# Kernel tuning notes

Hardware: AMD Instinct MI355X
Metric: run time of the kernel (lower is better)

Reference implementation:

```python
import jax, jax.numpy as jnp
import numpy as np

N_NODES = 50000
N_EDGES = 800000
N_GRAPHS = 1024
H = 128          # hidden_dim
L = 5            # n_conv_layers
NODE_IN = 4
EDGE_IN = 41
N_TARGETS = 3
EPS = 1e-5


def _ln(x, g, b):
    m = jnp.mean(x, axis=-1, keepdims=True)
    v = jnp.var(x, axis=-1, keepdims=True)
    return (x - m) / jnp.sqrt(v + EPS) * g + b


def setup_inputs() -> dict:
    key = jax.random.key(0)
    ks = jax.random.split(key, 24)
    w = lambda k, shp: (jax.random.normal(k, shp, dtype=jnp.float32) * 0.05)
    inp = {
        "atom_fea": jax.random.normal(ks[0], (N_NODES, NODE_IN), dtype=jnp.float32),
        "nbr_fea": jax.random.normal(ks[1], (N_EDGES, EDGE_IN), dtype=jnp.float32),
        "nbr_idx": jax.random.randint(ks[2], (N_EDGES, 2), 0, N_NODES, dtype=jnp.int32),
        "batch_mapping": jnp.sort(jax.random.randint(ks[3], (N_NODES,), 0, N_GRAPHS, dtype=jnp.int32)),
        # node embedding: Linear(4->H) + LayerNorm + SiLU
        "emb_w": w(ks[4], (NODE_IN, H)), "emb_b": jnp.zeros((H,), jnp.float32),
        "emb_ln_g": jnp.ones((H,), jnp.float32), "emb_ln_b": jnp.zeros((H,), jnp.float32),
        # edge embedding: Linear(41->H) + SiLU
        "edge_w": w(ks[5], (EDGE_IN, H)), "edge_b": jnp.zeros((H,), jnp.float32),
        # conv layers: Linear(2H->2H), SiLU, Linear(2H->H), SiLU; stacked over L
        "conv_w1": w(ks[6], (L, 2 * H, 2 * H)), "conv_b1": jnp.zeros((L, 2 * H), jnp.float32),
        "conv_w2": w(ks[7], (L, 2 * H, H)), "conv_b2": jnp.zeros((L, H), jnp.float32),
        "ln_g": jnp.ones((L, H), jnp.float32), "ln_b": jnp.zeros((L, H), jnp.float32),
        # output head
        "out_w1": w(ks[8], (H, H)), "out_b1": jnp.zeros((H,), jnp.float32),
        "out_w2": w(ks[9], (H, H // 2)), "out_b2": jnp.zeros((H // 2,), jnp.float32),
        "out_w3": w(ks[10], (H // 2, N_TARGETS)), "out_b3": jnp.zeros((N_TARGETS,), jnp.float32),
    }
    return inp


def reference(atom_fea, nbr_fea, nbr_idx, batch_mapping,
              emb_w, emb_b, emb_ln_g, emb_ln_b, edge_w, edge_b,
              conv_w1, conv_b1, conv_w2, conv_b2, ln_g, ln_b,
              out_w1, out_b1, out_w2, out_b2, out_w3, out_b3):
    silu = jax.nn.silu
    # embeddings (dropout is eval-mode identity)
    x = silu(_ln(atom_fea @ emb_w + emb_b, emb_ln_g, emb_ln_b))      # [N, H]
    e = silu(nbr_fea @ edge_w + edge_b)                               # [E, H]
    src, dst = nbr_idx[:, 0], nbr_idx[:, 1]
    n = x.shape[0]
    # per-node incoming edge counts (same every layer)
    cnt = jax.ops.segment_sum(jnp.ones_like(dst, dtype=x.dtype), dst, num_segments=n)
    cnt = jnp.clip(cnt, 1.0)[:, None]
    for i in range(L):
        m = jnp.concatenate([x[src], e], axis=1)                      # [E, 2H] gather
        m = silu(m @ conv_w1[i] + conv_b1[i])                         # [E, 2H]
        m = silu(m @ conv_w2[i] + conv_b2[i])                         # [E, H]
        aggr = jax.ops.segment_sum(m, dst, num_segments=n) / cnt      # scatter-mean
        x = _ln(x + aggr, ln_g[i], ln_b[i])                           # residual + LN
    # graph-level mean pooling
    gcnt = jax.ops.segment_sum(jnp.ones((n,), x.dtype), batch_mapping, num_segments=N_GRAPHS)
    gcnt = jnp.clip(gcnt, 1.0)[:, None]
    crystal = jax.ops.segment_sum(x, batch_mapping, num_segments=N_GRAPHS) / gcnt  # [G, H]
    h = silu(crystal @ out_w1 + out_b1)
    h = silu(h @ out_w2 + out_b2)
    return h @ out_w3 + out_b3                                        # [G, n_targets]
```

## Files before the change

### kernel.cpp

```cpp
#include <hip/hip_runtime.h>
#include <hip/hip_bf16.h>
#include <math.h>

#define N_NODES 50000
#define N_EDGES 800000
#define N_GRAPHS 1024
#define HD 128
#define NLAYERS 5
#define EDGE_IN 41
#define NT 3
#define LN_EPS 1e-5f

typedef unsigned int uint;
typedef unsigned short ushort;
typedef __attribute__((ext_vector_type(8))) short short8;
typedef __attribute__((ext_vector_type(4))) float f32x4;

__device__ __forceinline__ float silu_f(float v) {
    return v * __builtin_amdgcn_rcpf(1.0f + __expf(-v));
}

__device__ __forceinline__ ushort f2bf(float f) {
    uint u = __float_as_uint(f);
    u = u + 0x7FFFu + ((u >> 16) & 1u);
    return (ushort)(u >> 16);
}

__device__ __forceinline__ short8 ld16(const ushort* p) {
    union { int4 i; short8 s; } u;
    u.i = *(const int4*)p;
    return u.s;
}

__device__ __forceinline__ f32x4 mfma16(short8 a, short8 b, f32x4 c) {
    return __builtin_amdgcn_mfma_f32_16x16x32_bf16(a, b, c, 0, 0, 0);
}

__device__ __forceinline__ void wave_lds_fence() {
    __asm__ volatile("s_waitcnt lgkmcnt(0)" ::: "memory");
}

__device__ __forceinline__ void cp16(const ushort* g, ushort* l) {
    __builtin_amdgcn_global_load_lds(
        (const __attribute__((address_space(1))) unsigned int*)g,
        (__attribute__((address_space(3))) unsigned int*)l, 16, 0, 0);
}

__device__ __forceinline__ void stage4k(ushort* lds, const ushort* g, int w, int L) {
#pragma unroll
    for (int i = 0; i < 2; ++i) {
        int f = w * 1024 + i * 512;
        cp16(g + f + L * 8, lds + f);
    }
}

__global__ void k_zero(float* __restrict__ p, int n) {
    int i = blockIdx.x * 256 + threadIdx.x;
    if (i < n) p[i] = 0.0f;
}

__global__ void k_swz_w1(const float* __restrict__ w1, ushort* __restrict__ w1s) {
    int i = blockIdx.x * 256 + threadIdx.x;
    int l = i >> 16;
    int r = i & 65535;
    int j = r & 7, L = (r >> 3) & 63, s = (r >> 9) & 7, c = (r >> 12) & 15;
    int k = 32 * s + ((L >> 4) & 3) * 8 + j;
    int n = 16 * c + (L & 15);
    w1s[i] = f2bf(w1[(size_t)l * 65536 + k * 256 + n]);
}
__global__ void k_swz_w2(const float* __restrict__ w2, ushort* __restrict__ w2s) {
    int i = blockIdx.x * 256 + threadIdx.x;
    int l = i >> 15;
    int r = i & 32767;
    int j = r & 7, L = (r >> 3) & 63, t = (r >> 9) & 7, s2 = (r >> 12) & 7;
    int k = 32 * s2 + ((L >> 4) & 3) * 8 + j;
    int n = 16 * t + (L & 15);
    w2s[i] = f2bf(w2[(size_t)l * 32768 + k * 128 + n]);
}

__global__ __launch_bounds__(128) void k_node_embed(
    const float* __restrict__ atom, const float* __restrict__ w,
    const float* __restrict__ b, const float* __restrict__ g,
    const float* __restrict__ bet, float* __restrict__ x, ushort* __restrict__ x_bf)
{
    int node = blockIdx.x;
    int h = threadIdx.x;
    float4 a = *(const float4*)(atom + (size_t)node * 4);
    float acc = b[h] + a.x * w[h] + a.y * w[HD + h] + a.z * w[2 * HD + h] + a.w * w[3 * HD + h];
    __shared__ float s1[2], s2[2];
    float sum = acc, sq = acc * acc;
    for (int off = 32; off > 0; off >>= 1) { sum += __shfl_down(sum, off); sq += __shfl_down(sq, off); }
    int wid = h >> 6, lane = h & 63;
    if (lane == 0) { s1[wid] = sum; s2[wid] = sq; }
    __syncthreads();
    float m = (s1[0] + s1[1]) * (1.0f / 128.0f);
    float v = (s2[0] + s2[1]) * (1.0f / 128.0f) - m * m;
    float y = (acc - m) * rsqrtf(v + LN_EPS) * g[h] + bet[h];
    y = silu_f(y);
    x[(size_t)node * HD + h] = y;
    x_bf[(size_t)node * HD + h] = f2bf(y);
}

#define ETILE 32
__global__ __launch_bounds__(128) void k_edge_embed(
    const float* __restrict__ fea, const float* __restrict__ w,
    const float* __restrict__ b, ushort* __restrict__ e_bf)
{
    __shared__ float sf[ETILE][EDGE_IN + 1];
    int e0 = blockIdx.x * ETILE;
    int tid = threadIdx.x;
    for (int i = tid; i < ETILE * EDGE_IN; i += 128) {
        int m = i / EDGE_IN, k = i % EDGE_IN;
        sf[m][k] = fea[(size_t)(e0 + m) * EDGE_IN + k];
    }
    __syncthreads();
    float bb = b[tid];
    float acc[ETILE];
#pragma unroll
    for (int m = 0; m < ETILE; m++) acc[m] = bb;
    for (int k = 0; k < EDGE_IN; k++) {
        float wk = w[k * HD + tid];
#pragma unroll
        for (int m = 0; m < ETILE; m++) acc[m] += sf[m][k] * wk;
    }
#pragma unroll
    for (int m = 0; m < ETILE; m++)
        e_bf[(size_t)(e0 + m) * HD + tid] = f2bf(silu_f(acc[m]));
}

__global__ void k_count(const int* __restrict__ nbr_idx, float* __restrict__ cnt) {
    int i = blockIdx.x * 256 + threadIdx.x;
    if (i < N_EDGES) atomicAdd(&cnt[nbr_idx[2 * i + 1]], 1.0f);
}
__global__ void k_gcount(const int* __restrict__ bm, float* __restrict__ gcnt) {
    int i = blockIdx.x * 256 + threadIdx.x;
    if (i < N_NODES) atomicAdd(&gcnt[bm[i]], 1.0f);
}

#define M1CP 40
__global__ __launch_bounds__(256) void k_conv_mfma(
    const ushort* __restrict__ x_bf, const ushort* __restrict__ e_bf,
    const int* __restrict__ nbr_idx,
    const ushort* __restrict__ w1s, const float* __restrict__ cb1,
    const ushort* __restrict__ w2s, const float* __restrict__ cb2,
    float* __restrict__ aggr)
{
    __shared__ __align__(16) ushort sW1[2][4096];
    __shared__ __align__(16) ushort sW2[2][4096];
    __shared__ __align__(16) ushort sM1[4][16 * M1CP];
    __shared__ int sDst[64];

    int tid = threadIdx.x;
    int w = tid >> 6;
    int L = tid & 63;
    int m = L & 15;
    int quad = L >> 4;
    int e0 = blockIdx.x * 64 + w * 16;

    if (L < 16) sDst[w * 16 + L] = nbr_idx[2 * (e0 + L) + 1];
    int src = nbr_idx[2 * (e0 + m)];

    const ushort* xr = x_bf + (size_t)src * HD + quad * 8;
    const ushort* er = e_bf + (size_t)(e0 + m) * HD + quad * 8;
    short8 af[8];
#pragma unroll
    for (int s = 0; s < 4; ++s) af[s] = ld16(xr + 32 * s);
#pragma unroll
    for (int s = 0; s < 4; ++s) af[4 + s] = ld16(er + 32 * s);

    f32x4 acc2[8];
#pragma unroll
    for (int t = 0; t < 8; ++t)
#pragma unroll
        for (int r = 0; r < 4; ++r) acc2[t][r] = 0.0f;

    ushort* sm = sM1[w];

    stage4k(sW1[0], w1s, w, L);
    stage4k(sW2[0], w2s, w, L);

    for (int p = 0; p < 16; ++p) {
        __syncthreads();
        if (p < 15) stage4k(sW1[(p + 1) & 1], w1s + (p + 1) * 4096, w, L);
        if ((p & 1) && (p >> 1) < 7)
            stage4k(sW2[((p >> 1) + 1) & 1], w2s + ((p >> 1) + 1) * 4096, w, L);

        f32x4 a1;
#pragma unroll
        for (int r = 0; r < 4; ++r) a1[r] = 0.0f;
        const ushort* wb = sW1[p & 1] + L * 8;
#pragma unroll
        for (int s = 0; s < 8; ++s)
            a1 = mfma16(af[s], ld16(wb + s * 512), a1);

        float bv = cb1[p * 16 + m];
        int hb = (p & 1) * 16;
#pragma unroll
        for (int r = 0; r < 4; ++r)
            sm[(quad * 4 + r) * M1CP + hb + m] = f2bf(silu_f(a1[r] + bv));

        if (p & 1) {
            wave_lds_fence();
            short8 a2 = ld16(sm + m * M1CP + quad * 8);
            const ushort* w2p = sW2[(p >> 1) & 1] + L * 8;
#pragma unroll
            for (int t = 0; t < 8; ++t)
                acc2[t] = mfma16(a2, ld16(w2p + t * 512), acc2[t]);
            wave_lds_fence();
        }
    }

#pragma unroll
    for (int t = 0; t < 8; ++t) {
        float bv = cb2[t * 16 + m];
#pragma unroll
        for (int r = 0; r < 4; ++r) {
            int dst = sDst[w * 16 + quad * 4 + r];
            atomicAdd(aggr + (size_t)dst * HD + t * 16 + m, silu_f(acc2[t][r] + bv));
        }
    }
}

__global__ __launch_bounds__(128) void k_post(
    const float* __restrict__ aggr, const float* __restrict__ cnt,
    const float* __restrict__ g, const float* __restrict__ bet,
    float* __restrict__ x, ushort* __restrict__ x_bf)
{
    int node = blockIdx.x;
    int h = threadIdx.x;
    float inv = __builtin_amdgcn_rcpf(fmaxf(cnt[node], 1.0f));
    float acc = x[(size_t)node * HD + h] + aggr[(size_t)node * HD + h] * inv;
    __shared__ float s1[2], s2[2];
    float sum = acc, sq = acc * acc;
    for (int off = 32; off > 0; off >>= 1) { sum += __shfl_down(sum, off); sq += __shfl_down(sq, off); }
    int wid = h >> 6, lane = h & 63;
    if (lane == 0) { s1[wid] = sum; s2[wid] = sq; }
    __syncthreads();
    float m = (s1[0] + s1[1]) * (1.0f / 128.0f);
    float v = (s2[0] + s2[1]) * (1.0f / 128.0f) - m * m;
    float y = (acc - m) * rsqrtf(v + LN_EPS) * g[h] + bet[h];
    x[(size_t)node * HD + h] = y;
    x_bf[(size_t)node * HD + h] = f2bf(y);
}

__global__ __launch_bounds__(128) void k_gaggr(
    const float* __restrict__ x, const int* __restrict__ bm,
    float* __restrict__ crystal)
{
    int node = blockIdx.x;
    int h = threadIdx.x;
    atomicAdd(&crystal[(size_t)bm[node] * HD + h], x[(size_t)node * HD + h]);
}

__global__ __launch_bounds__(128) void k_readout(
    const float* __restrict__ crystal, const float* __restrict__ gcnt,
    const float* __restrict__ w1, const float* __restrict__ b1,
    const float* __restrict__ w2, const float* __restrict__ b2,
    const float* __restrict__ w3, const float* __restrict__ b3,
    float* __restrict__ out)
{
    int gph = blockIdx.x;
    int t = threadIdx.x;
    __shared__ float sc[HD], sh1[HD], sh2[64];
    float inv = __builtin_amdgcn_rcpf(fmaxf(gcnt[gph], 1.0f));
    sc[t] = crystal[(size_t)gph * HD + t] * inv;
    __syncthreads();
    float acc = b1[t];
    for (int k = 0; k < HD; k++) acc += sc[k] * w1[k * HD + t];
    sh1[t] = silu_f(acc);
    __syncthreads();
    if (t < 64) {
        float a2 = b2[t];
        for (int k = 0; k < HD; k++) a2 += sh1[k] * w2[k * 64 + t];
        sh2[t] = silu_f(a2);
    }
    __syncthreads();
    if (t < NT) {
        float a3 = b3[t];
        for (int k = 0; k < 64; k++) a3 += sh2[k] * w3[k * NT + t];
        out[(size_t)gph * NT + t] = a3;
    }
}

extern "C" void kernel_launch(void* const* d_in, const int* in_sizes, int n_in,
                              void* d_out, int out_size, void* d_ws, size_t ws_size,
                              hipStream_t stream)
{
    const float* atom_fea = (const float*)d_in[0];
    const float* nbr_fea  = (const float*)d_in[1];
    const int*   nbr_idx  = (const int*)d_in[2];
    const int*   bm       = (const int*)d_in[3];
    const float* emb_w    = (const float*)d_in[4];
    const float* emb_b    = (const float*)d_in[5];
    const float* emb_ln_g = (const float*)d_in[6];
    const float* emb_ln_b = (const float*)d_in[7];
    const float* edge_w   = (const float*)d_in[8];
    const float* edge_b   = (const float*)d_in[9];
    const float* conv_w1  = (const float*)d_in[10];
    const float* conv_b1  = (const float*)d_in[11];
    const float* conv_w2  = (const float*)d_in[12];
    const float* conv_b2  = (const float*)d_in[13];
    const float* ln_g     = (const float*)d_in[14];
    const float* ln_b     = (const float*)d_in[15];
    const float* out_w1   = (const float*)d_in[16];
    const float* out_b1   = (const float*)d_in[17];
    const float* out_w2   = (const float*)d_in[18];
    const float* out_b2   = (const float*)d_in[19];
    const float* out_w3   = (const float*)d_in[20];
    const float* out_b3   = (const float*)d_in[21];
    float* out = (float*)d_out;

    char* base = (char*)d_ws;
    size_t off = 0;
    auto alloc = [&](size_t bytes) -> char* {
        char* p = base + off;
        off = (off + bytes + 255) & ~(size_t)255;
        return p;
    };
    float*  xbuf    = (float*) alloc((size_t)N_NODES * HD * 4);
    float*  aggr    = (float*) alloc((size_t)N_NODES * HD * 4);
    float*  cnt     = (float*) alloc((size_t)N_NODES * 4);
    float*  crystal = (float*) alloc((size_t)N_GRAPHS * HD * 4);
    float*  gcnt    = (float*) alloc((size_t)N_GRAPHS * 4);
    ushort* x_bf    = (ushort*)alloc((size_t)N_NODES * HD * 2);
    ushort* e_bf    = (ushort*)alloc((size_t)N_EDGES * HD * 2);
    ushort* w1s     = (ushort*)alloc((size_t)NLAYERS * 65536 * 2);
    ushort* w2s     = (ushort*)alloc((size_t)NLAYERS * 32768 * 2);

    k_swz_w1<<<(NLAYERS * 65536) / 256, 256, 0, stream>>>(conv_w1, w1s);
    k_swz_w2<<<(NLAYERS * 32768) / 256, 256, 0, stream>>>(conv_w2, w2s);

    int zn = N_NODES + N_GRAPHS * HD + N_GRAPHS + 128;
    k_zero<<<(zn + 255) / 256, 256, 0, stream>>>(cnt, zn);

    k_node_embed<<<N_NODES, 128, 0, stream>>>(atom_fea, emb_w, emb_b, emb_ln_g, emb_ln_b, xbuf, x_bf);
    k_edge_embed<<<N_EDGES / ETILE, 128, 0, stream>>>(nbr_fea, edge_w, edge_b, e_bf);
    k_count<<<N_EDGES / 256, 256, 0, stream>>>(nbr_idx, cnt);
    k_gcount<<<(N_NODES + 255) / 256, 256, 0, stream>>>(bm, gcnt);

    for (int l = 0; l < NLAYERS; ++l) {
        k_zero<<<(N_NODES * HD) / 256, 256, 0, stream>>>(aggr, N_NODES * HD);
        k_conv_mfma<<<N_EDGES / 64, 256, 0, stream>>>(
            x_bf, e_bf, nbr_idx,
            w1s + (size_t)l * 65536, conv_b1 + (size_t)l * 256,
            w2s + (size_t)l * 32768, conv_b2 + (size_t)l * 128,
            aggr);
        k_post<<<N_NODES, 128, 0, stream>>>(aggr, cnt, ln_g + (size_t)l * HD, ln_b + (size_t)l * HD, xbuf, x_bf);
    }

    k_gaggr<<<N_NODES, 128, 0, stream>>>(xbuf, bm, crystal);
    k_readout<<<N_GRAPHS, 128, 0, stream>>>(crystal, gcnt, out_w1, out_b1, out_w2, out_b2, out_w3, out_b3, out);
}
```

Baseline: 2.794 ms.

## Process 32 edges per wave to reuse weight fragments; fold aggr zeroing into post

Each wave now handles two 16-edge tiles, so every weight fragment loaded from LDS feeds two MFMAs. This halves LDS weight traffic and weight staging per edge, and the grid shrinks to N_EDGES/128 blocks. The per-layer zero kernel is removed: k_post clears aggr after reading it, and a single zero runs before the loop. Launch bounds now request 3 blocks per SM. The extra accumulators and fragments raise register pressure, which may lower occupancy or cause spills.

```diff
diff --git a/kernel.cpp b/kernel.cpp
--- a/kernel.cpp
+++ b/kernel.cpp
@@ -138,7 +138,7 @@
 }
 
 #define M1CP 40
-__global__ __launch_bounds__(256) void k_conv_mfma(
+__global__ __launch_bounds__(256, 3) void k_conv_mfma(
     const ushort* __restrict__ x_bf, const ushort* __restrict__ e_bf,
     const int* __restrict__ nbr_idx,
     const ushort* __restrict__ w1s, const float* __restrict__ cb1,
@@ -147,32 +147,38 @@
 {
     __shared__ __align__(16) ushort sW1[2][4096];
     __shared__ __align__(16) ushort sW2[2][4096];
-    __shared__ __align__(16) ushort sM1[4][16 * M1CP];
-    __shared__ int sDst[64];
+    __shared__ __align__(16) ushort sM1[4][32 * M1CP];
+    __shared__ int sDst[128];
 
     int tid = threadIdx.x;
     int w = tid >> 6;
     int L = tid & 63;
     int m = L & 15;
     int quad = L >> 4;
-    int e0 = blockIdx.x * 64 + w * 16;
-
-    if (L < 16) sDst[w * 16 + L] = nbr_idx[2 * (e0 + L) + 1];
-    int src = nbr_idx[2 * (e0 + m)];
-
-    const ushort* xr = x_bf + (size_t)src * HD + quad * 8;
-    const ushort* er = e_bf + (size_t)(e0 + m) * HD + quad * 8;
-    short8 af[8];
-#pragma unroll
-    for (int s = 0; s < 4; ++s) af[s] = ld16(xr + 32 * s);
-#pragma unroll
-    for (int s = 0; s < 4; ++s) af[4 + s] = ld16(er + 32 * s);
-
-    f32x4 acc2[8];
-#pragma unroll
-    for (int t = 0; t < 8; ++t)
-#pragma unroll
-        for (int r = 0; r < 4; ++r) acc2[t][r] = 0.0f;
+    int eb = blockIdx.x * 128;
+    int ew = eb + w * 32;
+
+    if (tid < 128) sDst[tid] = nbr_idx[2 * (eb + tid) + 1];
+
+    short8 af[2][8];
+#pragma unroll
+    for (int t = 0; t < 2; ++t) {
+        int src = nbr_idx[2 * (ew + t * 16 + m)];
+        const ushort* xr = x_bf + (size_t)src * HD + quad * 8;
+        const ushort* er = e_bf + (size_t)(ew + t * 16 + m) * HD + quad * 8;
+#pragma unroll
+        for (int s = 0; s < 4; ++s) af[t][s] = ld16(xr + 32 * s);
+#pragma unroll
+        for (int s = 0; s < 4; ++s) af[t][4 + s] = ld16(er + 32 * s);
+    }
+
+    f32x4 acc2[2][8];
+#pragma unroll
+    for (int t = 0; t < 2; ++t)
+#pragma unroll
+        for (int tt = 0; tt < 8; ++tt)
+#pragma unroll
+            for (int r = 0; r < 4; ++r) acc2[t][tt][r] = 0.0f;
 
     ushort* sm = sM1[w];
 
@@ -185,51 +191,66 @@
         if ((p & 1) && (p >> 1) < 7)
             stage4k(sW2[((p >> 1) + 1) & 1], w2s + ((p >> 1) + 1) * 4096, w, L);
 
-        f32x4 a1;
-#pragma unroll
-        for (int r = 0; r < 4; ++r) a1[r] = 0.0f;
+        f32x4 p0, p1;
+#pragma unroll
+        for (int r = 0; r < 4; ++r) { p0[r] = 0.0f; p1[r] = 0.0f; }
         const ushort* wb = sW1[p & 1] + L * 8;
 #pragma unroll
-        for (int s = 0; s < 8; ++s)
-            a1 = mfma16(af[s], ld16(wb + s * 512), a1);
+        for (int s = 0; s < 8; ++s) {
+            short8 wv = ld16(wb + s * 512);
+            p0 = mfma16(af[0][s], wv, p0);
+            p1 = mfma16(af[1][s], wv, p1);
+        }
 
         float bv = cb1[p * 16 + m];
         int hb = (p & 1) * 16;
 #pragma unroll
-        for (int r = 0; r < 4; ++r)
-            sm[(quad * 4 + r) * M1CP + hb + m] = f2bf(silu_f(a1[r] + bv));
+        for (int r = 0; r < 4; ++r) {
+            sm[(quad * 4 + r) * M1CP + hb + m]        = f2bf(silu_f(p0[r] + bv));
+            sm[(16 + quad * 4 + r) * M1CP + hb + m]   = f2bf(silu_f(p1[r] + bv));
+        }
 
         if (p & 1) {
             wave_lds_fence();
-            short8 a2 = ld16(sm + m * M1CP + quad * 8);
+            short8 a20 = ld16(sm + m * M1CP + quad * 8);
+            short8 a21 = ld16(sm + (16 + m) * M1CP + quad * 8);
             const ushort* w2p = sW2[(p >> 1) & 1] + L * 8;
 #pragma unroll
-            for (int t = 0; t < 8; ++t)
-                acc2[t] = mfma16(a2, ld16(w2p + t * 512), acc2[t]);
+            for (int tt = 0; tt < 8; ++tt) {
+                short8 bf = ld16(w2p + tt * 512);
+                acc2[0][tt] = mfma16(a20, bf, acc2[0][tt]);
+                acc2[1][tt] = mfma16(a21, bf, acc2[1][tt]);
+            }
             wave_lds_fence();
         }
     }
 
 #pragma unroll
-    for (int t = 0; t < 8; ++t) {
-        float bv = cb2[t * 16 + m];
-#pragma unroll
-        for (int r = 0; r < 4; ++r) {
-            int dst = sDst[w * 16 + quad * 4 + r];
-            atomicAdd(aggr + (size_t)dst * HD + t * 16 + m, silu_f(acc2[t][r] + bv));
+    for (int t = 0; t < 2; ++t) {
+#pragma unroll
+        for (int tt = 0; tt < 8; ++tt) {
+            float bv = cb2[tt * 16 + m];
+#pragma unroll
+            for (int r = 0; r < 4; ++r) {
+                int dst = sDst[w * 32 + t * 16 + quad * 4 + r];
+                atomicAdd(aggr + (size_t)dst * HD + tt * 16 + m,
+                          silu_f(acc2[t][tt][r] + bv));
+            }
         }
     }
 }
 
 __global__ __launch_bounds__(128) void k_post(
-    const float* __restrict__ aggr, const float* __restrict__ cnt,
+    float* __restrict__ aggr, const float* __restrict__ cnt,
     const float* __restrict__ g, const float* __restrict__ bet,
     float* __restrict__ x, ushort* __restrict__ x_bf)
 {
     int node = blockIdx.x;
     int h = threadIdx.x;
     float inv = __builtin_amdgcn_rcpf(fmaxf(cnt[node], 1.0f));
-    float acc = x[(size_t)node * HD + h] + aggr[(size_t)node * HD + h] * inv;
+    float av = aggr[(size_t)node * HD + h];
+    aggr[(size_t)node * HD + h] = 0.0f;
+    float acc = x[(size_t)node * HD + h] + av * inv;
     __shared__ float s1[2], s2[2];
     float sum = acc, sq = acc * acc;
     for (int off = 32; off > 0; off >>= 1) { sum += __shfl_down(sum, off); sq += __shfl_down(sq, off); }
@@ -330,6 +351,7 @@
     k_swz_w1<<<(NLAYERS * 65536) / 256, 256, 0, stream>>>(conv_w1, w1s);
     k_swz_w2<<<(NLAYERS * 32768) / 256, 256, 0, stream>>>(conv_w2, w2s);
 
+    k_zero<<<(N_NODES * HD) / 256, 256, 0, stream>>>(aggr, N_NODES * HD);
     int zn = N_NODES + N_GRAPHS * HD + N_GRAPHS + 128;
     k_zero<<<(zn + 255) / 256, 256, 0, stream>>>(cnt, zn);
 
@@ -339,8 +361,7 @@
     k_gcount<<<(N_NODES + 255) / 256, 256, 0, stream>>>(bm, gcnt);
 
     for (int l = 0; l < NLAYERS; ++l) {
-        k_zero<<<(N_NODES * HD) / 256, 256, 0, stream>>>(aggr, N_NODES * HD);
-        k_conv_mfma<<<N_EDGES / 64, 256, 0, stream>>>(
+        k_conv_mfma<<<N_EDGES / 128, 256, 0, stream>>>(
             x_bf, e_bf, nbr_idx,
             w1s + (size_t)l * 65536, conv_b1 + (size_t)l * 256,
             w2s + (size_t)l * 32768, conv_b2 + (size_t)l * 128,
```

Result: no change. 2.753 ms (-1.4%).
